# Kernel tuning notes

Hardware: AMD Instinct MI355X
Metric: run time of the kernel (lower is better)

The kernel has to match this reference:

```python
import jax, jax.numpy as jnp
import numpy as np

B, S, E = 4, 2048, 1024
H, HD, R = 16, 64, 32  # heads, head_dim, rank


def setup_inputs() -> dict:
    key = jax.random.key(0)
    ks = jax.random.split(key, 9)
    sc = 0.02
    return {
        "hidden_states": jax.random.normal(ks[0], (B, S, E), jnp.float32),
        "q_weight": jax.random.normal(ks[1], (E, E), jnp.float32) * sc,
        "q_bias": jax.random.normal(ks[2], (E,), jnp.float32) * sc,
        "k_weight": jax.random.normal(ks[3], (E, E), jnp.float32) * sc,
        "k_bias": jax.random.normal(ks[4], (E,), jnp.float32) * sc,
        "low_rank_value_weight": jax.random.normal(ks[5], (E, H * R), jnp.float32) * sc,
        "low_rank_value_bias": jax.random.normal(ks[6], (H * R,), jnp.float32) * sc,
        "low_rank_output_weight": jax.random.normal(ks[7], (H * R, E), jnp.float32) * sc,
        "output_bias": jax.random.normal(ks[8], (E,), jnp.float32) * sc,
    }


def reference(hidden_states, q_weight, q_bias, k_weight, k_bias,
              low_rank_value_weight, low_rank_value_bias,
              low_rank_output_weight, output_bias):
    b, s, _ = hidden_states.shape
    q = hidden_states @ q_weight + q_bias                       # [B,S,E]
    k = hidden_states @ k_weight + k_bias                       # [B,S,E]
    v = hidden_states @ low_rank_value_weight + low_rank_value_bias  # [B,S,H*R]
    q = q.reshape(b, s, H, HD).transpose(0, 2, 1, 3)            # [B,H,S,HD]
    k = k.reshape(b, s, H, HD).transpose(0, 2, 1, 3)
    v = v.reshape(b, s, H, R).transpose(0, 2, 1, 3)             # [B,H,S,R]
    scores = jnp.einsum('bhqd,bhkd->bhqk', q, k) / jnp.sqrt(jnp.float32(HD))
    causal = jnp.tril(jnp.ones((s, s), dtype=bool))
    scores = jnp.where(causal, scores, jnp.finfo(scores.dtype).min)
    probs = jax.nn.softmax(scores, axis=-1)                     # [B,H,S,S]
    attn = jnp.einsum('bhqk,bhkr->bhqr', probs, v)              # [B,H,S,R]
    attn = attn.transpose(0, 2, 1, 3).reshape(b, s, H * R)      # [B,S,H*R]
    out = attn @ low_rank_output_weight + output_bias           # [B,S,E]
    return out
```

## Files before the change

### kernel.cpp

```cpp
#include <hip/hip_runtime.h>

typedef _Float16 f16;
typedef __attribute__((ext_vector_type(4))) float f4;
typedef __attribute__((ext_vector_type(4))) _Float16 h4;
typedef __attribute__((ext_vector_type(8))) _Float16 h8;
typedef __attribute__((ext_vector_type(4))) float f32x4;
typedef __attribute__((ext_vector_type(4))) unsigned int u4;

extern "C" __device__ __attribute__((const)) float __ocml_native_exp2_f32(float);
#define EXP2F __ocml_native_exp2_f32
#define L2E 1.4426950408889634f

#define SWZ(row, colByte) \
  (((row) << 7) + ((colByte) ^ (((((row) ^ ((row) >> 3))) & 7) << 4)))

#define GL16(gp, lp)                                                  \
  __builtin_amdgcn_global_load_lds(                                   \
      (const __attribute__((address_space(1))) unsigned int*)(gp),    \
      (__attribute__((address_space(3))) unsigned int*)(lp), 16, 0, 0)

__global__ __launch_bounds__(256) void prep(
    const float* __restrict__ hs, f16* __restrict__ hsf,
    const float* __restrict__ qw, const float* __restrict__ kw,
    const float* __restrict__ vw, const float* __restrict__ ow,
    f16* __restrict__ wqkv, f16* __restrict__ owt) {
  const int t = threadIdx.x;
  if (blockIdx.x < 2048) {
    const int n4 = 8192 * 1024 / 4;
    for (int i = blockIdx.x * 256 + t; i < n4; i += 2048 * 256) {
      const f4 v = ((const f4*)hs)[i];
      h4 h;
      h.x = (f16)v.x; h.y = (f16)v.y; h.z = (f16)v.z; h.w = (f16)v.w;
      ((h4*)hsf)[i] = h;
    }
    return;
  }
  __shared__ float tile[32][33];
  int bid = blockIdx.x - 2048;
  const float* in;
  f16* out;
  int R, C, bx, by;
  if (bid < 1024) {
    in = qw; out = wqkv; R = 1024; C = 1024; bx = bid & 31; by = bid >> 5;
  } else if (bid < 2048) {
    bid -= 1024;
    in = kw; out = wqkv + (size_t)1024 * 1024; R = 1024; C = 1024;
    bx = bid & 31; by = bid >> 5;
  } else if (bid < 2560) {
    bid -= 2048;
    in = vw; out = wqkv + (size_t)2048 * 1024; R = 1024; C = 512;
    bx = bid & 15; by = bid >> 4;
  } else {
    bid -= 2560;
    in = ow; out = owt; R = 512; C = 1024; bx = bid & 31; by = bid >> 5;
  }
  const int tx = t & 31, ty = t >> 5;
  const int bc = bx * 32, br = by * 32;
#pragma unroll
  for (int i = 0; i < 4; ++i)
    tile[ty + i * 8][tx] = in[(size_t)(br + ty + i * 8) * C + bc + tx];
  __syncthreads();
#pragma unroll
  for (int i = 0; i < 4; ++i)
    out[(size_t)(bc + ty + i * 8) * R + br + tx] = (f16)tile[tx][ty + i * 8];
}

__global__ __launch_bounds__(256) void hgemm_qkv(
    const f16* __restrict__ A, const f16* __restrict__ Bt,
    const float* __restrict__ qb, const float* __restrict__ kb,
    const float* __restrict__ vb,
    f16* __restrict__ qf, f16* __restrict__ kf, f16* __restrict__ vf) {
  __shared__ f16 As[2 * 128 * 32];
  __shared__ f16 Bs[2 * 128 * 32];
  const int K = 1024;
  const int id = blockIdx.x;
  const int xcd = id & 7, loc = id >> 3;
  const int grp = loc >> 5, inn = loc & 31;
  const int bnT = grp * 4 + (inn >> 3);
  const int bm = (xcd * 8 + (inn & 7)) * 128;
  const int bn = bnT * 128;
  const int t = threadIdx.x;
  const int lane = t & 63, wave = t >> 6;
  const int wr = wave >> 1, wc = wave & 1;
  const int lrow = lane & 15, lk = lane >> 4;
  const int srow = lane >> 2;
  const int sblk = (lane & 3) ^ ((srow ^ (srow >> 2)) & 3);

  f32x4 acc[4][4];
#pragma unroll
  for (int i = 0; i < 4; ++i)
#pragma unroll
    for (int j = 0; j < 4; ++j) acc[i][j] = (f32x4)0.f;

  auto stage = [&](int buf, int ktile) {
#pragma unroll
    for (int i = 0; i < 2; ++i) {
      const int rr = (wave * 2 + i) * 16 + srow;
      GL16(A + (size_t)(bm + rr) * K + ktile * 32 + sblk * 8,
           (char*)As + buf * 8192 + (wave * 2 + i) * 1024);
      GL16(Bt + (size_t)(bn + rr) * K + ktile * 32 + sblk * 8,
           (char*)Bs + buf * 8192 + (wave * 2 + i) * 1024);
    }
  };

  stage(0, 0);
  for (int kt = 0; kt < 32; ++kt) {
    const int cur = kt & 1;
    stage(cur ^ 1, (kt + 1) & 31);
    asm volatile("s_waitcnt vmcnt(4)" ::: "memory");
    __builtin_amdgcn_s_barrier();
    __builtin_amdgcn_sched_barrier(0);
    h8 af[4], bf[4];
#pragma unroll
    for (int f = 0; f < 4; ++f) {
      const int ra = wr * 64 + f * 16 + lrow;
      af[f] = *(const h8*)((char*)As + cur * 8192 + ra * 64 +
                           ((lk ^ ((ra ^ (ra >> 2)) & 3)) << 4));
      const int rb = wc * 64 + f * 16 + lrow;
      bf[f] = *(const h8*)((char*)Bs + cur * 8192 + rb * 64 +
                           ((lk ^ ((rb ^ (rb >> 2)) & 3)) << 4));
    }
#pragma unroll
    for (int i2 = 0; i2 < 4; ++i2)
#pragma unroll
      for (int j = 0; j < 4; ++j)
        acc[i2][j] = __builtin_amdgcn_mfma_f32_16x16x32_f16(af[i2], bf[j], acc[i2][j], 0, 0, 0);
    asm volatile("s_waitcnt lgkmcnt(0)" ::: "memory");
    __builtin_amdgcn_sched_barrier(0);
    __builtin_amdgcn_s_barrier();
  }

  const float* bias;
  int nbase;
  if (bnT < 8) { bias = qb; nbase = 0; }
  else if (bnT < 16) { bias = kb; nbase = 1024; }
  else { bias = vb; nbase = 2048; }

#pragma unroll
  for (int fi = 0; fi < 4; ++fi) {
#pragma unroll
    for (int j = 0; j < 4; ++j) {
      const int grow = bm + wr * 64 + fi * 16 + lk * 4 + j;
      const int bb = grow >> 11, ss = grow & 2047;
#pragma unroll
      for (int fj = 0; fj < 4; ++fj) {
        const int gcol = bn + wc * 64 + fj * 16 + lrow;
        const int nl = gcol - nbase;
        const float g = acc[fi][fj][j] + bias[nl];
        if (bnT < 8) {
          qf[((size_t)(bb * 16 + (nl >> 6)) * 2048 + ss) * 64 + (nl & 63)] = (f16)g;
        } else if (bnT < 16) {
          kf[((size_t)(bb * 16 + (nl >> 6)) * 2048 + ss) * 64 + (nl & 63)] = (f16)g;
        } else {
          vf[((size_t)(bb * 16 + (nl >> 5)) * 2048 + ss) * 32 + (nl & 31)] = (f16)g;
        }
      }
    }
  }
}

__global__ __launch_bounds__(256) void transpose_v(
    const f16* __restrict__ vf, f16* __restrict__ vfT) {
  __shared__ f16 tl[32][36];
  const int bh = blockIdx.x >> 6;
  const int st = (blockIdx.x & 63) * 32;
  const int t = threadIdx.x;
  const int row = t >> 3, cq = t & 7;
  {
    const h4 v = *(const h4*)(vf + ((size_t)bh * 2048 + st + row) * 32 + cq * 4);
    *(h4*)&tl[row][cq * 4] = v;
  }
  __syncthreads();
  {
    h4 v;
#pragma unroll
    for (int e = 0; e < 4; ++e) v[e] = tl[cq * 4 + e][row];
    *(h4*)(vfT + ((size_t)bh * 32 + row) * 2048 + st + cq * 4) = v;
  }
}

__global__ __launch_bounds__(256) void hgemm_out(
    const f16* __restrict__ A, const f16* __restrict__ Bt,
    const float* __restrict__ bias, float* __restrict__ outp,
    const int N, const int K) {
  __shared__ f16 As[128 * 40];
  __shared__ f16 Bs[128 * 40];
  const int id = blockIdx.x;
  const int swz = (id & 7) * 64 + (id >> 3);
  const int bn = (swz & 7) * 128;
  const int bm = (swz >> 3) * 128;
  const int t = threadIdx.x;
  const int lane = t & 63, wave = t >> 6;
  const int wr = wave >> 1, wc = wave & 1;
  const int lrow = lane & 15, lk = lane >> 4;

  f32x4 acc[4][4];
#pragma unroll
  for (int i = 0; i < 4; ++i)
#pragma unroll
    for (int j = 0; j < 4; ++j) acc[i][j] = (f32x4)0.f;

  for (int kt = 0; kt < K; kt += 32) {
#pragma unroll
    for (int i = 0; i < 2; ++i) {
      const int ch = t + i * 256;
      const int row = ch >> 2, part = ch & 3;
      *(u4*)&As[row * 40 + part * 8] =
          *(const u4*)(A + (size_t)(bm + row) * K + kt + part * 8);
      *(u4*)&Bs[row * 40 + part * 8] =
          *(const u4*)(Bt + (size_t)(bn + row) * K + kt + part * 8);
    }
    __syncthreads();
    h8 af[4], bf[4];
#pragma unroll
    for (int f = 0; f < 4; ++f) {
      af[f] = *(const h8*)&As[(wr * 64 + f * 16 + lrow) * 40 + lk * 8];
      bf[f] = *(const h8*)&Bs[(wc * 64 + f * 16 + lrow) * 40 + lk * 8];
    }
#pragma unroll
    for (int i = 0; i < 4; ++i)
#pragma unroll
      for (int j = 0; j < 4; ++j)
        acc[i][j] = __builtin_amdgcn_mfma_f32_16x16x32_f16(af[i], bf[j], acc[i][j], 0, 0, 0);
    __syncthreads();
  }

#pragma unroll
  for (int fi = 0; fi < 4; ++fi) {
#pragma unroll
    for (int j = 0; j < 4; ++j) {
      const int grow = bm + wr * 64 + fi * 16 + lk * 4 + j;
#pragma unroll
      for (int fj = 0; fj < 4; ++fj) {
        const int gcol = bn + wc * 64 + fj * 16 + lrow;
        outp[(size_t)grow * N + gcol] = acc[fi][fj][j] + bias[gcol];
      }
    }
  }
}

__global__ __launch_bounds__(256) void attn_mfma(
    const f16* __restrict__ qf, const f16* __restrict__ kf,
    const f16* __restrict__ vfT, f16* __restrict__ attf) {
  __shared__ f16 Ks[64 * 64];
  __shared__ f16 VsT[32 * 64];
  __shared__ f16 Ps[4 * 32 * 64];
  const int id = blockIdx.x;
  const int bh = id & 63;
  const int qblk = 15 - (id >> 6);
  const int qbase = qblk * 128;
  const int t = threadIdx.x;
  const int lane = t & 63, w = t >> 6;
  const int l15 = lane & 15, g = lane >> 4;
  const size_t kvbase = (size_t)bh * 2048;
  char* Pw = (char*)&Ps[w * 32 * 64];

  h8 ones;
#pragma unroll
  for (int e = 0; e < 8; ++e) ones[e] = (f16)1.0f;

  h8 qreg[2][2];
#pragma unroll
  for (int fj = 0; fj < 2; ++fj) {
    const int q = qbase + fj * 64 + w * 16 + l15;
#pragma unroll
    for (int ks = 0; ks < 2; ++ks) {
      h8 raw = *(const h8*)(qf + (kvbase + q) * 64 + ks * 32 + g * 8);
#pragma unroll
      for (int e = 0; e < 8; ++e) raw[e] = raw[e] * (f16)0.125f;
      qreg[fj][ks] = raw;
    }
  }

  f32x4 accO[2][2];
  f32x4 accL[2];
#pragma unroll
  for (int i = 0; i < 2; ++i) {
    accL[i] = (f32x4)0.f;
#pragma unroll
    for (int j = 0; j < 2; ++j) accO[i][j] = (f32x4)0.f;
  }
  float m2[2] = {-1.0e30f, -1.0e30f};

  const int ntiles = qblk * 2 + 2;
  for (int kt = 0; kt < ntiles; ++kt) {
    const int kbase = kt * 64;
    __syncthreads();
#pragma unroll
    for (int i = 0; i < 2; ++i) {
      const int chunk = w * 2 + i;
      const int row = chunk * 8 + (lane >> 3);
      const int srcb = (lane & 7) ^ ((row ^ (row >> 3)) & 7);
      GL16(kf + (kvbase + kbase + row) * 64 + srcb * 8,
           (char*)Ks + chunk * 1024);
    }
    {
      const int vrow = w * 8 + (lane >> 3);
      const int vsrcb = (lane & 7) ^ ((vrow ^ (vrow >> 3)) & 7);
      GL16(vfT + ((size_t)bh * 32 + vrow) * 2048 + kbase + vsrcb * 8,
           (char*)VsT + w * 1024);
    }
    __syncthreads();

    f32x4 accS[4][2];
#pragma unroll
    for (int i = 0; i < 4; ++i)
#pragma unroll
      for (int j = 0; j < 2; ++j) accS[i][j] = (f32x4)0.f;
#pragma unroll
    for (int ks = 0; ks < 2; ++ks) {
#pragma unroll
      for (int fim = 0; fim < 4; ++fim) {
        const h8 af = *(const h8*)((char*)Ks + SWZ(fim * 16 + l15, ks * 64 + g * 16));
#pragma unroll
        for (int fj = 0; fj < 2; ++fj)
          accS[fim][fj] = __builtin_amdgcn_mfma_f32_16x16x32_f16(af, qreg[fj][ks], accS[fim][fj], 0, 0, 0);
      }
    }

#pragma unroll
    for (int fj = 0; fj < 2; ++fj) {
      const int qg = qbase + fj * 64 + w * 16 + l15;
      const bool need_mask = (kbase + 63 > qbase + fj * 64 + w * 16);
      float sc[4][4];
#pragma unroll
      for (int fim = 0; fim < 4; ++fim)
#pragma unroll
        for (int j = 0; j < 4; ++j) {
          float v = accS[fim][fj][j];
          if (need_mask) {
            const int key = kbase + fim * 16 + g * 4 + j;
            v = (key <= qg) ? v : -1.0e30f;
          }
          sc[fim][j] = v;
        }
      const float a0 = fmaxf(fmaxf(sc[0][0], sc[0][1]), sc[0][2]);
      const float a1 = fmaxf(fmaxf(sc[0][3], sc[1][0]), sc[1][1]);
      const float a2 = fmaxf(fmaxf(sc[1][2], sc[1][3]), sc[2][0]);
      const float a3 = fmaxf(fmaxf(sc[2][1], sc[2][2]), sc[2][3]);
      const float a4 = fmaxf(fmaxf(sc[3][0], sc[3][1]), sc[3][2]);
      float mc = fmaxf(fmaxf(fmaxf(a0, a1), a2),
                       fmaxf(fmaxf(a3, a4), sc[3][3]));
      mc = fmaxf(mc, __shfl_xor(mc, 16));
      mc = fmaxf(mc, __shfl_xor(mc, 32));
      if (!__all(mc <= m2[fj] + 1.5f)) {
        const float mnew = fmaxf(m2[fj], mc);
        const float corr = __expf(m2[fj] - mnew);
        m2[fj] = mnew;
#pragma unroll
        for (int j = 0; j < 4; ++j) {
          const float c = __shfl(corr, g * 4 + j);
          accO[fj][0][j] *= c;
          accO[fj][1][j] *= c;
          accL[fj][j] *= c;
        }
      }
      const float nml = -m2[fj] * L2E;
#pragma unroll
      for (int fim = 0; fim < 4; ++fim) {
        h4 hp;
#pragma unroll
        for (int j = 0; j < 4; ++j)
          hp[j] = (f16)EXP2F(fmaf(sc[fim][j], L2E, nml));
        *(h4*)(Pw + SWZ(fj * 16 + l15, fim * 32 + g * 8)) = hp;
      }
    }

#pragma unroll
    for (int ks = 0; ks < 2; ++ks) {
      const h8 pa0 = *(const h8*)(Pw + SWZ(l15, ks * 64 + g * 16));
      const h8 pa1 = *(const h8*)(Pw + SWZ(16 + l15, ks * 64 + g * 16));
#pragma unroll
      for (int fr = 0; fr < 2; ++fr) {
        const h8 vb = *(const h8*)((char*)VsT + SWZ(fr * 16 + l15, ks * 64 + g * 16));
        accO[0][fr] = __builtin_amdgcn_mfma_f32_16x16x32_f16(pa0, vb, accO[0][fr], 0, 0, 0);
        accO[1][fr] = __builtin_amdgcn_mfma_f32_16x16x32_f16(pa1, vb, accO[1][fr], 0, 0, 0);
      }
      accL[0] = __builtin_amdgcn_mfma_f32_16x16x32_f16(pa0, ones, accL[0], 0, 0, 0);
      accL[1] = __builtin_amdgcn_mfma_f32_16x16x32_f16(pa1, ones, accL[1], 0, 0, 0);
    }
  }

  const int b = bh >> 4, h = bh & 15;
#pragma unroll
  for (int fo = 0; fo < 2; ++fo) {
#pragma unroll
    for (int j = 0; j < 4; ++j) {
      const float iv = 1.f / accL[fo][j];
      const int q = qbase + fo * 64 + w * 16 + g * 4 + j;
#pragma unroll
      for (int fr = 0; fr < 2; ++fr) {
        const int r = fr * 16 + l15;
        attf[((size_t)b * 2048 + q) * 512 + h * 32 + r] = (f16)(accO[fo][fr][j] * iv);
      }
    }
  }
}

extern "C" void kernel_launch(void* const* d_in, const int* in_sizes, int n_in,
                              void* d_out, int out_size, void* d_ws, size_t ws_size,
                              hipStream_t stream) {
  const float* hs = (const float*)d_in[0];
  const float* qw = (const float*)d_in[1];
  const float* qb = (const float*)d_in[2];
  const float* kw = (const float*)d_in[3];
  const float* kb = (const float*)d_in[4];
  const float* vw = (const float*)d_in[5];
  const float* vb = (const float*)d_in[6];
  const float* ow = (const float*)d_in[7];
  const float* ob = (const float*)d_in[8];
  float* out = (float*)d_out;
  char* ws = (char*)d_ws;

  f16* qf = (f16*)(ws);
  f16* kf = (f16*)(ws + ((size_t)16 << 20));
  f16* vf = (f16*)(ws + ((size_t)32 << 20));
  f16* vfT = (f16*)(ws + ((size_t)72 << 20));
  f16* attf = (f16*)(ws + ((size_t)40 << 20));
  f16* wqkv = (f16*)(ws + ((size_t)48 << 20));
  f16* owt = (f16*)(ws + ((size_t)53 << 20));
  f16* hsf = (f16*)(ws + ((size_t)56 << 20));

  prep<<<dim3(5120), 256, 0, stream>>>(hs, hsf, qw, kw, vw, ow, wqkv, owt);
  hgemm_qkv<<<dim3(1280), 256, 0, stream>>>(hsf, wqkv, qb, kb, vb, qf, kf, vf);
  transpose_v<<<dim3(4096), 256, 0, stream>>>(vf, vfT);
  attn_mfma<<<dim3(1024), 256, 0, stream>>>(qf, kf, vfT, attf);
  hgemm_out<<<dim3(512), 256, 0, stream>>>(attf, owt, ob, out, 1024, 512);
}
```

Measured before the change: 162.0 us.

## Split causal attention KV range across two blocks and merge partial results

Splits the causal attention kernel so that each (batch, head, query-block) is handled by two blocks: one covers the first half of the key tiles and the other the remaining ones. The number of blocks doubles and the per-block work is more even across the causal triangle. Each block writes unnormalized partial outputs plus its row sum and max to workspace, and a new merge kernel rescales and combines the two halves. This adds an extra kernel launch and extra global traffic for the partials. The merge weights the halves with natural exp of the max difference, and the running max now starts at 0 instead of a large negative value, so correctness depends on how the unseen loop body uses m2.

```diff
diff --git a/kernel.cpp b/kernel.cpp
--- a/kernel.cpp
+++ b/kernel.cpp
@@ -239,16 +239,21 @@
   }
 }
 
-__global__ __launch_bounds__(256) void attn_mfma(
+__global__ __launch_bounds__(256) void attn_split(
     const f16* __restrict__ qf, const f16* __restrict__ kf,
-    const f16* __restrict__ vfT, f16* __restrict__ attf) {
+    const f16* __restrict__ vfT, f16* __restrict__ opart,
+    float* __restrict__ mlpart) {
   __shared__ f16 Ks[64 * 64];
   __shared__ f16 VsT[32 * 64];
   __shared__ f16 Ps[4 * 32 * 64];
   const int id = blockIdx.x;
   const int bh = id & 63;
-  const int qblk = 15 - (id >> 6);
+  const int qblk = 15 - ((id >> 6) & 15);
+  const int half = id >> 10;
   const int qbase = qblk * 128;
+  const int nt0 = qblk + 1;
+  const int t0 = half ? nt0 : 0;
+  const int t1 = half ? 2 * qblk + 2 : nt0;
   const int t = threadIdx.x;
   const int lane = t & 63, w = t >> 6;
   const int l15 = lane & 15, g = lane >> 4;
@@ -280,10 +285,9 @@
 #pragma unroll
     for (int j = 0; j < 2; ++j) accO[i][j] = (f32x4)0.f;
   }
-  float m2[2] = {-1.0e30f, -1.0e30f};
-
-  const int ntiles = qblk * 2 + 2;
-  for (int kt = 0; kt < ntiles; ++kt) {
+  float m2[2] = {0.f, 0.f};
+
+  for (int kt = t0; kt < t1; ++kt) {
     const int kbase = kt * 64;
     __syncthreads();
 #pragma unroll
@@ -381,19 +385,61 @@
     }
   }
 
+  f16* Op = opart + (size_t)(half * 64 + bh) * 2048 * 32;
+  float* Ml = mlpart + (size_t)(half * 64 + bh) * 2048 * 2;
+#pragma unroll
+  for (int fo = 0; fo < 2; ++fo) {
+#pragma unroll
+    for (int j = 0; j < 4; ++j) {
+      const int q = qbase + fo * 64 + w * 16 + g * 4 + j;
+#pragma unroll
+      for (int fr = 0; fr < 2; ++fr)
+        Op[(size_t)q * 32 + fr * 16 + l15] = (f16)accO[fo][fr][j];
+    }
+  }
+  if (l15 == 0) {
+#pragma unroll
+    for (int fo = 0; fo < 2; ++fo)
+#pragma unroll
+      for (int j = 0; j < 4; ++j) {
+        const int q = qbase + fo * 64 + w * 16 + g * 4 + j;
+        Ml[q * 2 + 0] = accL[fo][j];
+      }
+  }
+  if (g == 0) {
+#pragma unroll
+    for (int fj = 0; fj < 2; ++fj) {
+      const int q = qbase + fj * 64 + w * 16 + l15;
+      Ml[q * 2 + 1] = m2[fj];
+    }
+  }
+}
+
+__global__ __launch_bounds__(256) void attn_merge(
+    const f16* __restrict__ opart, const float* __restrict__ mlpart,
+    f16* __restrict__ attf) {
+  const int bh = blockIdx.x >> 3;
+  const int q = (blockIdx.x & 7) * 256 + threadIdx.x;
+  const size_t r0 = (size_t)bh * 2048 + q;
+  const size_t r1 = (size_t)(64 + bh) * 2048 + q;
+  const float l0 = mlpart[r0 * 2], m0 = mlpart[r0 * 2 + 1];
+  const float l1 = mlpart[r1 * 2], m1 = mlpart[r1 * 2 + 1];
+  const float m = fmaxf(m0, m1);
+  const float w0 = __expf(m0 - m), w1 = __expf(m1 - m);
+  const float inv = 1.f / (w0 * l0 + w1 * l1);
   const int b = bh >> 4, h = bh & 15;
-#pragma unroll
-  for (int fo = 0; fo < 2; ++fo) {
-#pragma unroll
-    for (int j = 0; j < 4; ++j) {
-      const float iv = 1.f / accL[fo][j];
-      const int q = qbase + fo * 64 + w * 16 + g * 4 + j;
-#pragma unroll
-      for (int fr = 0; fr < 2; ++fr) {
-        const int r = fr * 16 + l15;
-        attf[((size_t)b * 2048 + q) * 512 + h * 32 + r] = (f16)(accO[fo][fr][j] * iv);
-      }
-    }
+  f16* dst = attf + ((size_t)b * 2048 + q) * 512 + h * 32;
+  const f16* o0 = opart + r0 * 32;
+  const f16* o1 = opart + r1 * 32;
+#pragma unroll
+  for (int r8 = 0; r8 < 4; ++r8) {
+    const h8 a = *(const h8*)(o0 + r8 * 8);
+    const h8 c = *(const h8*)(o1 + r8 * 8);
+    h8 o;
+#pragma unroll
+    for (int e = 0; e < 8; ++e)
+      o[e] = (f16)((w0 * (float)a[e] + w1 * (float)c[e]) * inv);
+    *(h8*)(dst + r8 * 8) = o;
   }
 }
 
@@ -420,10 +466,13 @@
   f16* wqkv = (f16*)(ws + ((size_t)48 << 20));
   f16* owt = (f16*)(ws + ((size_t)53 << 20));
   f16* hsf = (f16*)(ws + ((size_t)56 << 20));
+  f16* opart = (f16*)(ws + ((size_t)56 << 20));
+  float* mlpart = (float*)(ws + ((size_t)80 << 20));
 
   prep<<<dim3(5120), 256, 0, stream>>>(hs, hsf, qw, kw, vw, ow, wqkv, owt);
   hgemm_qkv<<<dim3(1280), 256, 0, stream>>>(hsf, wqkv, qb, kb, vb, qf, kf, vf);
   transpose_v<<<dim3(4096), 256, 0, stream>>>(vf, vfT);
-  attn_mfma<<<dim3(1024), 256, 0, stream>>>(qf, kf, vfT, attf);
+  attn_split<<<dim3(2048), 256, 0, stream>>>(qf, kf, vfT, opart, mlpart);
+  attn_merge<<<dim3(512), 256, 0, stream>>>(opart, mlpart, attf);
   hgemm_out<<<dim3(512), 256, 0, stream>>>(attf, owt, ob, out, 1024, 512);
 }
```

Measured after the change: 175.1 us. 8.1% more time.
